# Performance work log

Hardware: AMD Instinct MI355X
Metric: run time of the kernel (lower is better)

The kernel has to match this reference:

```python
import jax, jax.numpy as jnp
import numpy as np

PAD_ID = 0


def setup_inputs() -> dict:
    key = jax.random.key(0)
    ks = jax.random.split(key, 14)
    B, S, T = 64, 128, 32
    E = H = 512
    V = 32000
    s = 0.02
    return {
        "trg_tokens": jax.random.randint(ks[0], (B, T), 0, V),
        "src_tokens": jax.random.randint(ks[1], (B, S), 0, V),
        "encoder_out": jax.random.normal(ks[2], (S, B, 2 * H), jnp.float32),
        "hidden": jax.random.normal(ks[3], (B, H), jnp.float32),
        "embed_w": jax.random.normal(ks[4], (V, E), jnp.float32) * s,
        "attn_W": jax.random.normal(ks[5], (H, 2 * H + H), jnp.float32) * s,
        "attn_b": jnp.zeros((H,), jnp.float32),
        "v": jax.random.uniform(ks[6], (H,), jnp.float32),
        "W_ih": jax.random.normal(ks[7], (3 * H, 2 * H + E), jnp.float32) * s,
        "W_hh": jax.random.normal(ks[8], (3 * H, H), jnp.float32) * s,
        "b_ih": jnp.zeros((3 * H,), jnp.float32),
        "b_hh": jnp.zeros((3 * H,), jnp.float32),
        "out_W": jax.random.normal(ks[9], (V, 2 * H + H + E), jnp.float32) * s,
        "out_b": jnp.zeros((V,), jnp.float32),
    }


def reference(trg_tokens, src_tokens, encoder_out, hidden, embed_w, attn_W,
              attn_b, v, W_ih, W_hh, b_ih, b_hh, out_W, out_b):
    # trg_tokens: [B, T], src_tokens: [B, S] (transposed inside, as in torch)
    B, T = trg_tokens.shape
    S = src_tokens.shape[1]
    H = hidden.shape[1]
    V = out_W.shape[0]

    # Embedding with padding_idx -> zero row at PAD_ID
    emb = embed_w.at[PAD_ID].set(0.0)
    mask = (src_tokens != PAD_ID)              # [B, S]
    enc_bt = jnp.transpose(encoder_out, (1, 0, 2))  # [B, S, 2H]
    trg = trg_tokens.T                          # [T, B]

    def step(h, tok):
        x = emb[tok]                            # [B, E]
        # Bahdanau attention
        hrep = jnp.broadcast_to(h[:, None, :], (B, S, H))
        feat = jnp.concatenate([hrep, enc_bt], axis=2)      # [B, S, H+2H]
        energy = jnp.tanh(feat @ attn_W.T + attn_b)          # [B, S, H]
        scores = jnp.einsum('bsd,d->bs', energy, v)          # [B, S]
        scores = jnp.where(mask, scores, -jnp.inf)
        attn = jax.nn.softmax(scores, axis=1)                # [B, S]
        weighted = jnp.einsum('bs,bsd->bd', attn, enc_bt)    # [B, 2H]
        # GRU cell (torch gate order: r, z, n)
        rnn_in = jnp.concatenate([x, weighted], axis=1)      # [B, E+2H]
        gi = rnn_in @ W_ih.T + b_ih                          # [B, 3H]
        gh = h @ W_hh.T + b_hh                               # [B, 3H]
        i_r, i_z, i_n = jnp.split(gi, 3, axis=1)
        h_r, h_z, h_n = jnp.split(gh, 3, axis=1)
        r = jax.nn.sigmoid(i_r + h_r)
        z = jax.nn.sigmoid(i_z + h_z)
        n = jnp.tanh(i_n + r * h_n)
        h_new = (1.0 - z) * n + z * h                        # [B, H]
        # Output projection over cat(output, weighted, x)
        out_feat = jnp.concatenate([h_new, weighted, x], axis=1)  # [B, 2H+H+E]
        logits = out_feat @ out_W.T + out_b                  # [B, V]
        return h_new, logits

    # Teacher forcing ratio = 1.0: inputs are trg[0:T-1]; outputs[0] stays zero
    _, logits_seq = jax.lax.scan(step, hidden, trg[:T - 1])  # [T-1, B, V]
    outputs = jnp.concatenate(
        [jnp.zeros((1, B, V), logits_seq.dtype), logits_seq], axis=0)
    return outputs
```

## Files before the change

kernel.cpp:

```cpp
#include <hip/hip_runtime.h>

typedef __attribute__((ext_vector_type(4))) float f32x4;
typedef __attribute__((ext_vector_type(2))) float f32x2;
typedef __attribute__((ext_vector_type(8))) short s16x8;
typedef __attribute__((ext_vector_type(4))) short s16x4;

#define B_ 64
#define S_ 128
#define T_ 32
#define H_ 512
#define V_ 32000
#define NTILES 2000

#define SY_TILE 32
#define SY_SLOT 64

__device__ __forceinline__ unsigned short f2bf(float f) {
  union { float f; unsigned u; } x; x.f = f;
  unsigned r = x.u + 0x7FFFu + ((x.u >> 16) & 1u);
  return (unsigned short)(r >> 16);
}
__device__ __forceinline__ float bf2f(unsigned short u) {
  union { unsigned u; float f; } x; x.u = ((unsigned)u) << 16; return x.f;
}
__device__ __forceinline__ float fast_tanh(float x) {
  float e = __expf(2.0f * x);
  return 1.0f - 2.0f / (e + 1.0f);
}
__device__ __forceinline__ float fast_sig(float x) {
  return 1.0f / (1.0f + __expf(-x));
}
__device__ __forceinline__ void gload16(const void* g, void* l) {
  __builtin_amdgcn_global_load_lds(
      (const __attribute__((address_space(1))) void*)g,
      (__attribute__((address_space(3))) void*)l, 16, 0, 0);
}
__device__ __forceinline__ void gload16nt(const void* g, void* l) {
  __builtin_amdgcn_global_load_lds(
      (const __attribute__((address_space(1))) void*)g,
      (__attribute__((address_space(3))) void*)l, 16, 0, 2);
}

__device__ __forceinline__ unsigned ald(const unsigned* p) {
  return __hip_atomic_load(p, __ATOMIC_RELAXED, __HIP_MEMORY_SCOPE_AGENT);
}
__device__ __forceinline__ void ast(unsigned* p, unsigned v) {
  __hip_atomic_store(p, v, __ATOMIC_RELAXED, __HIP_MEMORY_SCOPE_AGENT);
}
__device__ __forceinline__ void astf(float* p, float v) {
  union { unsigned u; float f; } x; x.f = v; ast((unsigned*)p, x.u);
}

__device__ __forceinline__ void phase_sync(unsigned* sync, int bid,
                                           unsigned st_ph, int nmask,
                                           unsigned wt_ph) {
  __syncthreads();
  if (threadIdx.x == 0)
    __hip_atomic_store(&sync[SY_SLOT + bid], st_ph, __ATOMIC_RELAXED,
                       __HIP_MEMORY_SCOPE_AGENT);
  if (threadIdx.x < 64) {
    const unsigned* p = &sync[SY_SLOT + (threadIdx.x & nmask)];
    while (ald(p) < wt_ph) __builtin_amdgcn_s_sleep(1);
  }
  __syncthreads();
}

template <int OUTBF>
__global__ __launch_bounds__(256) void big_gemm_k(
    const unsigned short* __restrict__ A, int lda,
    const unsigned short* __restrict__ W, const float* __restrict__ bias,
    void* __restrict__ Cv, int Mv, int N, int K) {
  __shared__ unsigned short As[128 * 32];
  __shared__ unsigned short Bs[128 * 32];
  const int t = threadIdx.x;
  const int wave = t >> 6, lane = t & 63;
  const int m0 = blockIdx.x * 128, n0 = blockIdx.y * 128;
  const int wm = (wave & 1) * 64, wn = (wave >> 1) * 64;
  const int fr = lane & 15, fq = lane >> 4;

  f32x4 acc[4][4];
#pragma unroll
  for (int i = 0; i < 4; ++i)
#pragma unroll
    for (int j = 0; j < 4; ++j) acc[i][j] = (f32x4){0.f, 0.f, 0.f, 0.f};

  const int g = (((lane & 3) ^ ((lane >> 3) & 3))) * 8;
  const size_t a_g0 = (size_t)(m0 + wave * 32 + (lane >> 2)) * lda + g;
  const size_t b_g0 = (size_t)(n0 + wave * 32 + (lane >> 2)) * K + g;
  unsigned short* As_w = As + wave * 1024;
  unsigned short* Bs_w = Bs + wave * 1024;
  const int sl = (fq ^ ((fr >> 1) & 3)) * 8;

  for (int kk = 0; kk < K; kk += 32) {
    gload16(A + a_g0 + kk, As_w);
    gload16(A + a_g0 + (size_t)16 * lda + kk, As_w + 512);
    gload16(W + b_g0 + kk, Bs_w);
    gload16(W + b_g0 + (size_t)16 * K + kk, Bs_w + 512);
    __syncthreads();
    s16x8 af[4], bfr[4];
#pragma unroll
    for (int f = 0; f < 4; ++f) {
      af[f] = *(const s16x8*)(As + (wm + f * 16 + fr) * 32 + sl);
      bfr[f] = *(const s16x8*)(Bs + (wn + f * 16 + fr) * 32 + sl);
    }
#pragma unroll
    for (int fm = 0; fm < 4; ++fm)
#pragma unroll
      for (int fn = 0; fn < 4; ++fn)
        acc[fm][fn] = __builtin_amdgcn_mfma_f32_16x16x32_bf16(af[fm], bfr[fn],
                                                              acc[fm][fn], 0, 0, 0);
    __syncthreads();
  }

#pragma unroll
  for (int fn = 0; fn < 4; ++fn) {
    int col = n0 + wn + fn * 16 + fr;
    float bv = bias[col];
#pragma unroll
    for (int fm = 0; fm < 4; ++fm) {
      int rb = m0 + wm + fm * 16 + fq * 4;
#pragma unroll
      for (int i = 0; i < 4; ++i) {
        int r = rb + i;
        if (r < Mv) {
          if (OUTBF)
            ((unsigned short*)Cv)[(size_t)r * N + col] = f2bf(acc[fm][fn][i] + bv);
          else
            ((float*)Cv)[(size_t)r * N + col] = acc[fm][fn][i] + bv;
        }
      }
    }
  }
}

__global__ __launch_bounds__(512) void fused_k(
    float* __restrict__ h, unsigned short* __restrict__ hbf_step,
    float* __restrict__ hgh_step, const unsigned short* __restrict__ Wcomb,
    const unsigned short* __restrict__ encp_bf,
    const unsigned short* __restrict__ enc_bf, const float* __restrict__ v,
    const int* __restrict__ src_tok, const unsigned short* __restrict__ Ww,
    const unsigned short* __restrict__ gix, const float* __restrict__ b_hh,
    unsigned short* __restrict__ Abf, const unsigned short* __restrict__ outW,
    const float* __restrict__ out_b, float* __restrict__ out,
    unsigned* __restrict__ sync) {
  __shared__ __align__(16) char smem[62464];
  __shared__ unsigned sh_idx;
  const int t = threadIdx.x;
  const int lane = t & 63, w = t >> 6;
  const int fr = lane & 15, fq = lane >> 4;

  if (blockIdx.x < 64) {
    unsigned short* Asm = (unsigned short*)smem;
    unsigned short* Wsm = (unsigned short*)(smem + 9216);
    unsigned short* Wp1 = (unsigned short*)(smem + 16128);
    float* gsm = (float*)(smem + 49408);
    float* sc = (float*)(smem + 61696);
    const int j = blockIdx.x;
    const int ar = t >> 3, ak = (t & 7) * 8;
    const int p1_n0 = j * 32;
    const int rowt_p1 = w & 3, colt_p1 = w >> 2;

#pragma unroll
    for (int c = 0; c < 4; ++c) {
      int id = t * 4 + c;
      int r = id >> 6, cc = id & 63;
      s16x8 wv = *(const s16x8*)(Wcomb + (size_t)(p1_n0 + r) * 512 + cc * 8);
      *(s16x8*)(Wp1 + r * 520 + cc * 8) = wv;
    }
    __syncthreads();

    for (int step = 0; step < 31; ++step) {
      const unsigned short* hbfS = hbf_step + (size_t)step * 64 * 512;
      unsigned short* hbfS1 = hbf_step + (size_t)(step + 1) * 64 * 512;
      float* hghS = hgh_step + (size_t)step * 64 * 2048;
      const unsigned ph = 3u * step;

      {
        s16x8 pa[8];
#pragma unroll
        for (int p = 0; p < 8; ++p)
          pa[p] = *(const s16x8*)(hbfS + ar * 512 + p * 64 + ak);
        f32x4 acc = {0.f, 0.f, 0.f, 0.f};
#pragma unroll
        for (int it = 0; it < 8; ++it) {
          *(s16x8*)(Asm + ar * 72 + ak) = pa[it];
          __syncthreads();
          s16x8 a0 = *(const s16x8*)(Asm + (rowt_p1 * 16 + fr) * 72 + fq * 8);
          s16x8 a1 = *(const s16x8*)(Asm + (rowt_p1 * 16 + fr) * 72 + 32 + fq * 8);
          s16x8 b0 =
              *(const s16x8*)(Wp1 + (colt_p1 * 16 + fr) * 520 + it * 64 + fq * 8);
          s16x8 b1 = *(const s16x8*)(Wp1 + (colt_p1 * 16 + fr) * 520 + it * 64 +
                                     32 + fq * 8);
          acc = __builtin_amdgcn_mfma_f32_16x16x32_bf16(a0, b0, acc, 0, 0, 0);
          acc = __builtin_amdgcn_mfma_f32_16x16x32_bf16(a1, b1, acc, 0, 0, 0);
          __syncthreads();
        }
        int col = p1_n0 + colt_p1 * 16 + fr;
#pragma unroll
        for (int i = 0; i < 4; ++i)
          astf(&hghS[(rowt_p1 * 16 + fq * 4 + i) * 2048 + col], acc[i]);
      }
      phase_sync(sync, j, ph + 1, 15, ph + 1);

      {
        const int b = j;
        const float* hp = hghS + (size_t)b * 2048;
        float vh[8], hh[8];
        {
          f32x4 v0 = *(const f32x4*)(v + lane * 8);
          f32x4 v1 = *(const f32x4*)(v + lane * 8 + 4);
          f32x4 h0 = *(const f32x4*)(hp + lane * 8);
          f32x4 h1 = *(const f32x4*)(hp + lane * 8 + 4);
#pragma unroll
          for (int q = 0; q < 4; ++q) {
            vh[q] = v0[q]; vh[4 + q] = v1[q];
            hh[q] = h0[q]; hh[4 + q] = h1[q];
          }
        }
        for (int s = w * 16; s < w * 16 + 16; ++s) {
          s16x8 e =
              *(const s16x8*)(encp_bf + (size_t)(b * 128 + s) * 512 + lane * 8);
          float p = 0.f;
#pragma unroll
          for (int q = 0; q < 8; ++q)
            p += vh[q] * fast_tanh(hh[q] + bf2f((unsigned short)e[q]));
          for (int m = 32; m; m >>= 1) p += __shfl_xor(p, m);
          if (lane == 0)
            sc[s] = (src_tok[b * 128 + s] != 0) ? p : -__builtin_inff();
        }
        __syncthreads();
        if (t < 64) {
          float a0 = sc[t], a1 = sc[t + 64];
          float mx = fmaxf(a0, a1);
          for (int m = 32; m; m >>= 1) mx = fmaxf(mx, __shfl_xor(mx, m));
          float e0 = __expf(a0 - mx), e1 = __expf(a1 - mx);
          float ssum = e0 + e1;
          for (int m = 32; m; m >>= 1) ssum += __shfl_xor(ssum, m);
          float inv = 1.0f / ssum;
          sc[t] = e0 * inv;
          sc[t + 64] = e1 * inv;
        }
        __syncthreads();
        const int d = t * 2;
        float w0 = 0.f, w1 = 0.f;
#pragma unroll 16
        for (int s = 0; s < 128; ++s) {
          float a = sc[s];
          unsigned u = *(const unsigned*)(enc_bf + (size_t)(b * 128 + s) * 1024 + d);
          union { unsigned u; float f; } lo, hi;
          lo.u = u << 16; hi.u = u & 0xffff0000u;
          w0 += a * lo.f; w1 += a * hi.f;
        }
        unsigned pk = ((unsigned)f2bf(w1) << 16) | (unsigned)f2bf(w0);
        ast((unsigned*)(Abf + (size_t)(step * 64 + b) * 2048 + 512 + d), pk);
      }
      phase_sync(sync, j, ph + 2, 63, ph + 2);

      if (j < 32) {
        const int d0 = j * 16;
        const int r0 = step * 64;
        const int rowt = (w < 4) ? w : (w - 4);
        const int wgate = ar >> 4, wdr = ar & 15;
        const unsigned short* wwrow =
            Ww + (size_t)(wgate * 512 + d0 + wdr) * 1024 + ak;
        const unsigned short* abrow = Abf + (size_t)(r0 + ar) * 2048 + 512 + ak;
        s16x8 pa[8], pw[8];
#pragma unroll
        for (int p = 0; p < 8; ++p) {
          pa[p] = *(const s16x8*)(abrow + p * 64);
          if (t < 384) pw[p] = *(const s16x8*)(wwrow + p * 64);
        }
        f32x4 acc0 = {0.f, 0.f, 0.f, 0.f}, acc1 = {0.f, 0.f, 0.f, 0.f};
#pragma unroll
        for (int it = 0; it < 16; ++it) {
          *(s16x8*)(Asm + ar * 72 + ak) = pa[it & 7];
          if (t < 384) *(s16x8*)(Wsm + ar * 72 + ak) = pw[it & 7];
          __syncthreads();
          if (it < 8) {
            pa[it] = *(const s16x8*)(abrow + (it + 8) * 64);
            if (t < 384) pw[it] = *(const s16x8*)(wwrow + (it + 8) * 64);
          }
          s16x8 a0 = *(const s16x8*)(Asm + (rowt * 16 + fr) * 72 + fq * 8);
          s16x8 a1 = *(const s16x8*)(Asm + (rowt * 16 + fr) * 72 + 32 + fq * 8);
          if (w < 4) {
            s16x8 b0 = *(const s16x8*)(Wsm + fr * 72 + fq * 8);
            s16x8 b1 = *(const s16x8*)(Wsm + fr * 72 + 32 + fq * 8);
            s16x8 c0 = *(const s16x8*)(Wsm + (32 + fr) * 72 + fq * 8);
            s16x8 c1 = *(const s16x8*)(Wsm + (32 + fr) * 72 + 32 + fq * 8);
            acc0 = __builtin_amdgcn_mfma_f32_16x16x32_bf16(a0, b0, acc0, 0, 0, 0);
            acc0 = __builtin_amdgcn_mfma_f32_16x16x32_bf16(a1, b1, acc0, 0, 0, 0);
            acc1 = __builtin_amdgcn_mfma_f32_16x16x32_bf16(a0, c0, acc1, 0, 0, 0);
            acc1 = __builtin_amdgcn_mfma_f32_16x16x32_bf16(a1, c1, acc1, 0, 0, 0);
          } else {
            s16x8 b0 = *(const s16x8*)(Wsm + (16 + fr) * 72 + fq * 8);
            s16x8 b1 = *(const s16x8*)(Wsm + (16 + fr) * 72 + 32 + fq * 8);
            acc0 = __builtin_amdgcn_mfma_f32_16x16x32_bf16(a0, b0, acc0, 0, 0, 0);
            acc0 = __builtin_amdgcn_mfma_f32_16x16x32_bf16(a1, b1, acc0, 0, 0, 0);
          }
          __syncthreads();
        }
        {
          const int colt0 = (w < 4) ? 0 : 1;
#pragma unroll
          for (int i = 0; i < 4; ++i) {
            int row = rowt * 16 + fq * 4 + i;
            gsm[row * 48 + colt0 * 16 + fr] =
                acc0[i] +
                bf2f(gix[(size_t)(r0 + row) * 1536 + colt0 * 512 + d0 + fr]);
          }
          if (w < 4) {
#pragma unroll
            for (int i = 0; i < 4; ++i) {
              int row = rowt * 16 + fq * 4 + i;
              gsm[row * 48 + 32 + fr] =
                  acc1[i] + bf2f(gix[(size_t)(r0 + row) * 1536 + 1024 + d0 + fr]);
            }
          }
        }
        __syncthreads();
        {
          int e = t * 2;
          int b = e >> 4, dd = e & 15, d = d0 + dd;
          float hv2[2];
          unsigned short hb2[2];
#pragma unroll
          for (int k = 0; k < 2; ++k) {
            float ir = gsm[b * 48 + dd + k];
            float iz = gsm[b * 48 + 16 + dd + k];
            float inn = gsm[b * 48 + 32 + dd + k];
            float hr = hghS[b * 2048 + 512 + d + k] + b_hh[d + k];
            float hz = hghS[b * 2048 + 1024 + d + k] + b_hh[512 + d + k];
            float hn = hghS[b * 2048 + 1536 + d + k] + b_hh[1024 + d + k];
            float r = fast_sig(ir + hr);
            float z = fast_sig(iz + hz);
            float n = fast_tanh(inn + r * hn);
            hv2[k] = (1.0f - z) * n + z * h[b * 512 + d + k];
            hb2[k] = f2bf(hv2[k]);
          }
          h[b * 512 + d] = hv2[0];
          h[b * 512 + d + 1] = hv2[1];
          unsigned pk = ((unsigned)hb2[1] << 16) | (unsigned)hb2[0];
          ast((unsigned*)(hbfS1 + b * 512 + d), pk);
          ast((unsigned*)(Abf + (size_t)(r0 + b) * 2048 + d), pk);
        }
      }
      phase_sync(sync, j, ph + 3, 31, ph + 3);
    }
  }

  unsigned short* As2 = (unsigned short*)smem;
  unsigned short* Bs2 = (unsigned short*)(smem + 16384);
  const int wr = (w >> 2) * 64, wc = (w & 3) * 64;

  int rowA[2], cgA[2], rowB[4], cgB[4];
#pragma unroll
  for (int c = 0; c < 2; ++c) {
    int id = (w * 2 + c) * 64 + lane;
    rowA[c] = id >> 3;
    cgA[c] = ((id & 7) - rowA[c]) & 7;
  }
#pragma unroll
  for (int c = 0; c < 4; ++c) {
    int id = (w * 4 + c) * 64 + lane;
    rowB[c] = id >> 3;
    cgB[c] = ((id & 7) - rowB[c]) & 7;
  }

  for (;;) {
    __syncthreads();
    if (t == 0)
      sh_idx = __hip_atomic_fetch_add(&sync[SY_TILE], 1u, __ATOMIC_RELAXED,
                                      __HIP_MEMORY_SCOPE_AGENT);
    __syncthreads();
    unsigned idx = sh_idx;
    if (idx >= NTILES) break;
    int mb = idx / 125;
    int nt = idx - mb * 125;
    int gate = mb * 2 + 1;
    if (gate > 30) gate = 30;
    unsigned need = 3u * gate + 3u;
    if (w == 0) {
      const unsigned* p = &sync[SY_SLOT + (lane & 31)];
      while (ald(p) < need) __builtin_amdgcn_s_sleep(16);
    }
    __syncthreads();

    const int m0 = mb * 128, n0 = nt * 256;
    f32x4 acc[4][4];
#pragma unroll
    for (int i = 0; i < 4; ++i)
#pragma unroll
      for (int jj = 0; jj < 4; ++jj) acc[i][jj] = (f32x4){0.f, 0.f, 0.f, 0.f};

    for (int kk = 0; kk < 2048; kk += 64) {
#pragma unroll
      for (int c = 0; c < 2; ++c)
        gload16(Abf + (size_t)(m0 + rowA[c]) * 2048 + kk + cgA[c] * 8,
                As2 + (w * 2 + c) * 512);
#pragma unroll
      for (int c = 0; c < 4; ++c)
        gload16nt(outW + (size_t)(n0 + rowB[c]) * 2048 + kk + cgB[c] * 8,
                  Bs2 + (w * 4 + c) * 512);
      __syncthreads();
#pragma unroll
      for (int kh = 0; kh < 2; ++kh) {
        int cg = kh * 4 + fq;
        s16x8 af[4], bf_[4];
#pragma unroll
        for (int i = 0; i < 4; ++i) {
          int rr = wr + i * 16 + fr;
          af[i] = *(const s16x8*)(As2 + rr * 64 + (((cg + rr) & 7) * 8));
        }
#pragma unroll
        for (int jj = 0; jj < 4; ++jj) {
          int rr = wc + jj * 16 + fr;
          bf_[jj] = *(const s16x8*)(Bs2 + rr * 64 + (((cg + rr) & 7) * 8));
        }
#pragma unroll
        for (int i = 0; i < 4; ++i)
#pragma unroll
          for (int jj = 0; jj < 4; ++jj)
            acc[i][jj] = __builtin_amdgcn_mfma_f32_16x16x32_bf16(
                af[i], bf_[jj], acc[i][jj], 0, 0, 0);
      }
      __syncthreads();
    }

#pragma unroll
    for (int jj = 0; jj < 4; ++jj) {
      int col = n0 + wc + jj * 16 + fr;
      float bv = out_b[col];
#pragma unroll
      for (int i = 0; i < 4; ++i) {
        int rb = m0 + wr + i * 16 + fq * 4;
#pragma unroll
        for (int ii = 0; ii < 4; ++ii) {
          int r = rb + ii;
          if (r < 1984) out[(size_t)(r + 64) * V_ + col] = acc[i][jj][ii] + bv;
        }
      }
    }
  }
}

__global__ __launch_bounds__(256) void cast_bf16_k(const float* __restrict__ src,
                                                   unsigned short* __restrict__ dst,
                                                   int n4) {
  int i = blockIdx.x * 256 + threadIdx.x;
  if (i >= n4) return;
  f32x4 f = *(const f32x4*)(src + (size_t)i * 4);
  s16x4 o;
#pragma unroll
  for (int q = 0; q < 4; ++q) o[q] = (short)f2bf(f[q]);
  *(s16x4*)(dst + (size_t)i * 4) = o;
}

__global__ __launch_bounds__(256) void enc_cast_k(const float* __restrict__ enc,
                                                  unsigned short* __restrict__ dst) {
  int i = blockIdx.x * 256 + threadIdx.x;
  int n = i * 4;
  int row = n >> 10, d = n & 1023;
  int s = row & (S_ - 1), b = row >> 7;
  f32x4 f = *(const f32x4*)(enc + ((size_t)s * B_ + b) * 1024 + d);
  s16x4 o;
#pragma unroll
  for (int q = 0; q < 4; ++q) o[q] = (short)f2bf(f[q]);
  *(s16x4*)(dst + (size_t)row * 1024 + d) = o;
}

__global__ __launch_bounds__(256) void build_wcomb_k(const float* __restrict__ aW,
                                                     const float* __restrict__ whh,
                                                     unsigned short* __restrict__ dst) {
  int idx = (blockIdx.x * 256 + threadIdx.x) * 4;
  int n = idx >> 9, k = idx & 511;
  const float* src = (n < 512) ? (aW + (size_t)n * 1536 + k)
                               : (whh + (size_t)(n - 512) * 512 + k);
  f32x4 f = *(const f32x4*)src;
  s16x4 o;
#pragma unroll
  for (int q = 0; q < 4; ++q) o[q] = (short)f2bf(f[q]);
  *(s16x4*)(dst + idx) = o;
}

__global__ __launch_bounds__(256) void build_wenc_k(const float* __restrict__ aW,
                                                    unsigned short* __restrict__ dst) {
  int idx = (blockIdx.x * 256 + threadIdx.x) * 4;
  int n = idx >> 10, k = idx & 1023;
  f32x4 f = *(const f32x4*)(aW + (size_t)n * 1536 + 512 + k);
  s16x4 o;
#pragma unroll
  for (int q = 0; q < 4; ++q) o[q] = (short)f2bf(f[q]);
  *(s16x4*)(dst + idx) = o;
}

__global__ __launch_bounds__(256) void build_wxw_k(const float* __restrict__ wih,
                                                   unsigned short* __restrict__ wx,
                                                   unsigned short* __restrict__ ww) {
  int flat = blockIdx.x * 256 + threadIdx.x;
  int n = flat / 384, c4 = (flat % 384) * 4;
  f32x4 f = *(const f32x4*)(wih + (size_t)n * 1536 + c4);
  s16x4 o;
#pragma unroll
  for (int q = 0; q < 4; ++q) o[q] = (short)f2bf(f[q]);
  if (c4 < 512)
    *(s16x4*)(wx + (size_t)n * 512 + c4) = o;
  else
    *(s16x4*)(ww + (size_t)n * 1024 + (c4 - 512)) = o;
}

__global__ __launch_bounds__(256) void hcast_k(const float* __restrict__ hidden,
                                               unsigned short* __restrict__ hbf0) {
  int i = blockIdx.x * 256 + threadIdx.x;
  f32x2 f = *(const f32x2*)(hidden + (size_t)i * 2);
  unsigned pk = ((unsigned)f2bf(f[1]) << 16) | (unsigned)f2bf(f[0]);
  *(unsigned*)(hbf0 + (size_t)i * 2) = pk;
}

__global__ __launch_bounds__(256) void xgather_k(const int* __restrict__ trg,
                                                 const float* __restrict__ embed,
                                                 unsigned short* __restrict__ Abf) {
  int row = blockIdx.x;
  int tt = row >> 6, b = row & 63;
  int tok = trg[b * T_ + tt];
  int d = threadIdx.x * 2;
  unsigned pk = 0;
  if (tok != 0) {
    f32x2 f = *(const f32x2*)(embed + (size_t)tok * H_ + d);
    pk = ((unsigned)f2bf(f[1]) << 16) | (unsigned)f2bf(f[0]);
  }
  *(unsigned*)(Abf + (size_t)row * 2048 + 1536 + d) = pk;
}

extern "C" void kernel_launch(void* const* d_in, const int* in_sizes, int n_in,
                              void* d_out, int out_size, void* d_ws, size_t ws_size,
                              hipStream_t stream) {
  const int* trg = (const int*)d_in[0];
  const int* srt = (const int*)d_in[1];
  const float* enc = (const float*)d_in[2];
  const float* hidden = (const float*)d_in[3];
  const float* embed = (const float*)d_in[4];
  const float* attn_W = (const float*)d_in[5];
  const float* attn_b = (const float*)d_in[6];
  const float* vv = (const float*)d_in[7];
  const float* W_ih = (const float*)d_in[8];
  const float* W_hh = (const float*)d_in[9];
  const float* b_ih = (const float*)d_in[10];
  const float* b_hh = (const float*)d_in[11];
  const float* out_W = (const float*)d_in[12];
  const float* out_b = (const float*)d_in[13];
  float* out = (float*)d_out;

  char* ws = (char*)d_ws;
  size_t off = 0;
  auto alloc = [&](size_t bytes) {
    size_t o = off;
    off += (bytes + 255) & ~(size_t)255;
    return ws + o;
  };

  unsigned short* outW_bf = (unsigned short*)alloc((size_t)V_ * 2048 * 2);
  unsigned short* Abf = (unsigned short*)alloc((size_t)2048 * 2048 * 2);
  unsigned short* enc_bf = (unsigned short*)alloc((size_t)B_ * S_ * 1024 * 2);
  unsigned short* encp_bf = (unsigned short*)alloc((size_t)B_ * S_ * 512 * 2);
  unsigned short* gix_bf = (unsigned short*)alloc((size_t)1984 * 1536 * 2);
  unsigned short* Wcomb = (unsigned short*)alloc((size_t)2048 * 512 * 2);
  unsigned short* Wenc = (unsigned short*)alloc((size_t)512 * 1024 * 2);
  unsigned short* Wx = (unsigned short*)alloc((size_t)1536 * 512 * 2);
  unsigned short* Ww = (unsigned short*)alloc((size_t)1536 * 1024 * 2);
  float* hgh_step = (float*)alloc((size_t)31 * B_ * 2048 * 4);
  unsigned short* hbf_step = (unsigned short*)alloc((size_t)32 * B_ * H_ * 2);
  float* h = (float*)alloc((size_t)B_ * H_ * 4);
  unsigned* syncb = (unsigned*)alloc(8192);

  hipMemsetAsync(out, 0, (size_t)B_ * V_ * 4, stream);
  hipMemsetAsync(syncb, 0, 8192, stream);
  hipMemsetAsync(Abf + (size_t)1984 * 2048, 0, (size_t)64 * 2048 * 2, stream);
  hipMemcpyAsync(h, hidden, (size_t)B_ * H_ * 4, hipMemcpyDeviceToDevice, stream);

  cast_bf16_k<<<(V_ * 2048 / 4 + 255) / 256, 256, 0, stream>>>(out_W, outW_bf,
                                                               V_ * 2048 / 4);
  build_wcomb_k<<<2048 * 512 / 4 / 256, 256, 0, stream>>>(attn_W, W_hh, Wcomb);
  build_wenc_k<<<512 * 1024 / 4 / 256, 256, 0, stream>>>(attn_W, Wenc);
  build_wxw_k<<<1536 * 384 / 256, 256, 0, stream>>>(W_ih, Wx, Ww);
  hcast_k<<<64, 256, 0, stream>>>(hidden, hbf_step);
  enc_cast_k<<<B_ * S_ * 1024 / 4 / 256, 256, 0, stream>>>(enc, enc_bf);
  xgather_k<<<1984, 256, 0, stream>>>(trg, embed, Abf);

  big_gemm_k<1><<<dim3(64, 4), 256, 0, stream>>>(enc_bf, 1024, Wenc, attn_b,
                                                 encp_bf, B_ * S_, 512, 1024);
  big_gemm_k<1><<<dim3(16, 12), 256, 0, stream>>>(Abf + 1536, 2048, Wx, b_ih,
                                                  gix_bf, 1984, 1536, 512);

  fused_k<<<256, 512, 0, stream>>>(h, hbf_step, hgh_step, Wcomb, encp_bf, enc_bf,
                                   vv, srt, Ww, gix_bf, b_hh, Abf, outW_bf, out_b,
                                   out, syncb);
}
```

Baseline: 1.484 ms.

## Double-buffer LDS tiles in recurrent GEMMs and preload GRU weights into registers

Switches the per-step hidden-projection and GRU input-gate GEMM loops to ping-pong LDS buffers, so the next K-slice is written while the current one is consumed, dropping one barrier per iteration. The 16 slices of the GRU weight rows are loaded once into registers before the step loop instead of being re-fetched from global memory every timestep. The shared-memory layout is repacked to 64KB, with the tile index moved into the top word of smem. This raises register pressure (32 s16x8 registers per thread) and could hurt occupancy or cause spills.

```diff
diff --git a/kernel.cpp b/kernel.cpp
--- a/kernel.cpp
+++ b/kernel.cpp
@@ -143,18 +143,19 @@
     unsigned short* __restrict__ Abf, const unsigned short* __restrict__ outW,
     const float* __restrict__ out_b, float* __restrict__ out,
     unsigned* __restrict__ sync) {
-  __shared__ __align__(16) char smem[62464];
-  __shared__ unsigned sh_idx;
+  __shared__ __align__(16) char smem[65536];
   const int t = threadIdx.x;
   const int lane = t & 63, w = t >> 6;
   const int fr = lane & 15, fq = lane >> 4;
 
   if (blockIdx.x < 64) {
-    unsigned short* Asm = (unsigned short*)smem;
-    unsigned short* Wsm = (unsigned short*)(smem + 9216);
-    unsigned short* Wp1 = (unsigned short*)(smem + 16128);
-    float* gsm = (float*)(smem + 49408);
-    float* sc = (float*)(smem + 61696);
+    unsigned short* A0 = (unsigned short*)smem;
+    unsigned short* A1 = (unsigned short*)(smem + 9216);
+    unsigned short* W0 = (unsigned short*)(smem + 18432);
+    unsigned short* W1 = (unsigned short*)(smem + 25344);
+    unsigned short* Wp1 = (unsigned short*)(smem + 32256);
+    float* gsm = (float*)smem;
+    float* sc = (float*)(smem + 12288);
     const int j = blockIdx.x;
     const int ar = t >> 3, ak = (t & 7) * 8;
     const int p1_n0 = j * 32;
@@ -167,6 +168,17 @@
       s16x8 wv = *(const s16x8*)(Wcomb + (size_t)(p1_n0 + r) * 512 + cc * 8);
       *(s16x8*)(Wp1 + r * 520 + cc * 8) = wv;
     }
+
+    const int rowt = (w < 4) ? w : (w - 4);
+    const int wgate = ar >> 4, wdr = ar & 15;
+    const int d0 = j * 16;
+    const unsigned short* wwrow =
+        Ww + (size_t)(wgate * 512 + d0 + wdr) * 1024 + ak;
+    s16x8 pwreg[16];
+    if (j < 32 && t < 384) {
+#pragma unroll
+      for (int p = 0; p < 16; ++p) pwreg[p] = *(const s16x8*)(wwrow + p * 64);
+    }
     __syncthreads();
 
     for (int step = 0; step < 31; ++step) {
@@ -180,13 +192,17 @@
 #pragma unroll
         for (int p = 0; p < 8; ++p)
           pa[p] = *(const s16x8*)(hbfS + ar * 512 + p * 64 + ak);
+        *(s16x8*)(A0 + ar * 72 + ak) = pa[0];
+        __syncthreads();
         f32x4 acc = {0.f, 0.f, 0.f, 0.f};
 #pragma unroll
         for (int it = 0; it < 8; ++it) {
-          *(s16x8*)(Asm + ar * 72 + ak) = pa[it];
-          __syncthreads();
-          s16x8 a0 = *(const s16x8*)(Asm + (rowt_p1 * 16 + fr) * 72 + fq * 8);
-          s16x8 a1 = *(const s16x8*)(Asm + (rowt_p1 * 16 + fr) * 72 + 32 + fq * 8);
+          unsigned short* bufR = (it & 1) ? A1 : A0;
+          unsigned short* bufW = (it & 1) ? A0 : A1;
+          s16x8 a0 = *(const s16x8*)(bufR + (rowt_p1 * 16 + fr) * 72 + fq * 8);
+          s16x8 a1 =
+              *(const s16x8*)(bufR + (rowt_p1 * 16 + fr) * 72 + 32 + fq * 8);
+          if (it < 7) *(s16x8*)(bufW + ar * 72 + ak) = pa[it + 1];
           s16x8 b0 =
               *(const s16x8*)(Wp1 + (colt_p1 * 16 + fr) * 520 + it * 64 + fq * 8);
           s16x8 b1 = *(const s16x8*)(Wp1 + (colt_p1 * 16 + fr) * 520 + it * 64 +
@@ -257,43 +273,39 @@
       phase_sync(sync, j, ph + 2, 63, ph + 2);
 
       if (j < 32) {
-        const int d0 = j * 16;
         const int r0 = step * 64;
-        const int rowt = (w < 4) ? w : (w - 4);
-        const int wgate = ar >> 4, wdr = ar & 15;
-        const unsigned short* wwrow =
-            Ww + (size_t)(wgate * 512 + d0 + wdr) * 1024 + ak;
         const unsigned short* abrow = Abf + (size_t)(r0 + ar) * 2048 + 512 + ak;
-        s16x8 pa[8], pw[8];
-#pragma unroll
-        for (int p = 0; p < 8; ++p) {
-          pa[p] = *(const s16x8*)(abrow + p * 64);
-          if (t < 384) pw[p] = *(const s16x8*)(wwrow + p * 64);
-        }
+        s16x8 pa[16];
+#pragma unroll
+        for (int p = 0; p < 16; ++p) pa[p] = *(const s16x8*)(abrow + p * 64);
+        *(s16x8*)(A0 + ar * 72 + ak) = pa[0];
+        if (t < 384) *(s16x8*)(W0 + ar * 72 + ak) = pwreg[0];
+        __syncthreads();
         f32x4 acc0 = {0.f, 0.f, 0.f, 0.f}, acc1 = {0.f, 0.f, 0.f, 0.f};
 #pragma unroll
         for (int it = 0; it < 16; ++it) {
-          *(s16x8*)(Asm + ar * 72 + ak) = pa[it & 7];
-          if (t < 384) *(s16x8*)(Wsm + ar * 72 + ak) = pw[it & 7];
-          __syncthreads();
-          if (it < 8) {
-            pa[it] = *(const s16x8*)(abrow + (it + 8) * 64);
-            if (t < 384) pw[it] = *(const s16x8*)(wwrow + (it + 8) * 64);
+          unsigned short* aR = (it & 1) ? A1 : A0;
+          unsigned short* wR = (it & 1) ? W1 : W0;
+          unsigned short* aW = (it & 1) ? A0 : A1;
+          unsigned short* wW = (it & 1) ? W0 : W1;
+          s16x8 a0 = *(const s16x8*)(aR + (rowt * 16 + fr) * 72 + fq * 8);
+          s16x8 a1 = *(const s16x8*)(aR + (rowt * 16 + fr) * 72 + 32 + fq * 8);
+          if (it < 15) {
+            *(s16x8*)(aW + ar * 72 + ak) = pa[it + 1];
+            if (t < 384) *(s16x8*)(wW + ar * 72 + ak) = pwreg[it + 1];
           }
-          s16x8 a0 = *(const s16x8*)(Asm + (rowt * 16 + fr) * 72 + fq * 8);
-          s16x8 a1 = *(const s16x8*)(Asm + (rowt * 16 + fr) * 72 + 32 + fq * 8);
           if (w < 4) {
-            s16x8 b0 = *(const s16x8*)(Wsm + fr * 72 + fq * 8);
-            s16x8 b1 = *(const s16x8*)(Wsm + fr * 72 + 32 + fq * 8);
-            s16x8 c0 = *(const s16x8*)(Wsm + (32 + fr) * 72 + fq * 8);
-            s16x8 c1 = *(const s16x8*)(Wsm + (32 + fr) * 72 + 32 + fq * 8);
+            s16x8 b0 = *(const s16x8*)(wR + fr * 72 + fq * 8);
+            s16x8 b1 = *(const s16x8*)(wR + fr * 72 + 32 + fq * 8);
+            s16x8 c0 = *(const s16x8*)(wR + (32 + fr) * 72 + fq * 8);
+            s16x8 c1 = *(const s16x8*)(wR + (32 + fr) * 72 + 32 + fq * 8);
             acc0 = __builtin_amdgcn_mfma_f32_16x16x32_bf16(a0, b0, acc0, 0, 0, 0);
             acc0 = __builtin_amdgcn_mfma_f32_16x16x32_bf16(a1, b1, acc0, 0, 0, 0);
             acc1 = __builtin_amdgcn_mfma_f32_16x16x32_bf16(a0, c0, acc1, 0, 0, 0);
             acc1 = __builtin_amdgcn_mfma_f32_16x16x32_bf16(a1, c1, acc1, 0, 0, 0);
           } else {
-            s16x8 b0 = *(const s16x8*)(Wsm + (16 + fr) * 72 + fq * 8);
-            s16x8 b1 = *(const s16x8*)(Wsm + (16 + fr) * 72 + 32 + fq * 8);
+            s16x8 b0 = *(const s16x8*)(wR + (16 + fr) * 72 + fq * 8);
+            s16x8 b1 = *(const s16x8*)(wR + (16 + fr) * 72 + 32 + fq * 8);
             acc0 = __builtin_amdgcn_mfma_f32_16x16x32_bf16(a0, b0, acc0, 0, 0, 0);
             acc0 = __builtin_amdgcn_mfma_f32_16x16x32_bf16(a1, b1, acc0, 0, 0, 0);
           }
@@ -350,6 +362,7 @@
 
   unsigned short* As2 = (unsigned short*)smem;
   unsigned short* Bs2 = (unsigned short*)(smem + 16384);
+  unsigned* shp = (unsigned*)(smem + 65532);
   const int wr = (w >> 2) * 64, wc = (w & 3) * 64;
 
   int rowA[2], cgA[2], rowB[4], cgB[4];
@@ -369,10 +382,10 @@
   for (;;) {
     __syncthreads();
     if (t == 0)
-      sh_idx = __hip_atomic_fetch_add(&sync[SY_TILE], 1u, __ATOMIC_RELAXED,
-                                      __HIP_MEMORY_SCOPE_AGENT);
+      *shp = __hip_atomic_fetch_add(&sync[SY_TILE], 1u, __ATOMIC_RELAXED,
+                                    __HIP_MEMORY_SCOPE_AGENT);
     __syncthreads();
-    unsigned idx = sh_idx;
+    unsigned idx = *shp;
     if (idx >= NTILES) break;
     int mb = idx / 125;
     int nt = idx - mb * 125;
```

Result: faster. 1.441 ms (-2.9%).
